# Kernel tuning notes

Hardware: AMD Instinct MI355X
Metric: run time of the kernel (lower is better)

## Reference

```python
import jax, jax.numpy as jnp
import numpy as np
from itertools import permutations

NUM_LAYERS = 3
K = 5  # fixed node degree -> every Hungarian sub-problem is 5x5
# one-hot permutation tensor: P1H[p, r, c] = 1 iff permutation p assigns row r -> col c
PERMS = np.array(list(permutations(range(K))), dtype=np.int32)          # [120, K]
P1H = (PERMS[:, :, None] == np.arange(K)[None, None, :]).astype(np.float32)  # [120, K, K]


def _mlp(x, W1, b1, W2, b2):
    # 2-layer MLP with ReLU (repo's MLP(in, hid, out, 2))
    return jax.nn.relu(x @ W1 + b1) @ W2 + b2


def _sinkhorn(src, itera):
    s = jax.nn.softmax(src, axis=1)  # row-max subtraction is built in
    for i in range(itera):
        s = s / jnp.sum(s, axis=i % 2, keepdims=True)
    return jnp.nan_to_num(s)


def _masked_softmax(src):
    s1 = jnp.nan_to_num(jax.nn.softmax(src, axis=1))
    s2 = jnp.nan_to_num(jax.nn.softmax(src, axis=0))
    return (s1 + s2) * 0.5


def setup_inputs() -> dict:
    key = jax.random.key(0)
    ks = jax.random.split(key, 12)
    n1 = n2 = 1024
    hid = 64
    adj1 = jax.random.randint(ks[0], (n1, K), 0, n1)
    adj2 = jax.random.randint(ks[1], (n2, K), 0, n2)
    # adjacency matrices consistent with the neighbor lists
    G1 = jnp.zeros((n1, n1), jnp.float32).at[jnp.arange(n1)[:, None], adj1].set(1.0)
    G2 = jnp.zeros((n2, n2), jnp.float32).at[jnp.arange(n2)[:, None], adj2].set(1.0)
    s = 0.1
    return {
        'G1': G1, 'G2': G2, 'adj1': adj1, 'adj2': adj2,
        'ro_W1': jax.random.normal(ks[2], (NUM_LAYERS, 1, hid), jnp.float32) * s,
        'ro_b1': jax.random.normal(ks[3], (NUM_LAYERS, hid), jnp.float32) * s,
        'ro_W2': jax.random.normal(ks[4], (NUM_LAYERS, hid, 1), jnp.float32) * s,
        'ro_b2': jax.random.normal(ks[5], (NUM_LAYERS, 1), jnp.float32) * s,
        'fin_W1': jax.random.normal(ks[6], (1, hid), jnp.float32) * s,
        'fin_b1': jax.random.normal(ks[7], (hid,), jnp.float32) * s,
        'fin_W2': jax.random.normal(ks[8], (hid, 1), jnp.float32) * s,
        'fin_b2': jax.random.normal(ks[9], (1,), jnp.float32) * s,
    }


def reference(G1, G2, adj1, adj2, ro_W1, ro_b1, ro_W2, ro_b2, fin_W1, fin_b1, fin_W2, fin_b2):
    n1 = G1.shape[0]
    n2 = G2.shape[0]
    d1 = jnp.sum(G1, axis=1)
    d2 = jnp.sum(G2, axis=1)
    ttheta = jnp.mean(d1)
    # S[i, j, 0] = -|d1[i] - d2[j]|
    S = -jnp.abs(d1[:, None] - d2[None, :])[..., None]  # [n1, n2, 1]
    p1h = jnp.asarray(P1H)
    for li in range(NUM_LAYERS):
        Wn = _sinkhorn(_mlp(S / ttheta, ro_W1[li], ro_b1[li], ro_W2[li], ro_b2[li]).squeeze(-1), 5)
        W = jnp.log(Wn * (n1 * 1.5))
        W = jnp.where(jnp.isneginf(W), jnp.float32(-1e12), W)
        W = jnp.where(jnp.isposinf(W), jnp.float32(1e12), W)
        Wd = jax.lax.stop_gradient(W)  # matches W.detach().numpy()
        # small[a, b, r, c] = Wd[adj1[a, r], adj2[b, c]]  -> [n1, n2, K, K]
        small = jnp.transpose(Wd[adj1][:, :, adj2], (0, 2, 1, 3))
        # exact linear_sum_assignment(-small): maximize sum over the K! permutations
        scores = jnp.einsum('abrc,prc->abp', small, p1h)  # [n1, n2, 120]
        X1 = jnp.max(scores, axis=-1)                      # [n1, n2]
        S = X1[..., None]
    out = _masked_softmax(_mlp(S, fin_W1, fin_b1, fin_W2, fin_b2).squeeze(-1))
    return out
```

## Files before the change

### kernel.cpp

```cpp
#include <hip/hip_runtime.h>
#include <math.h>

#define N 1024
#define NB 256
#define KD 5
#define SL 8


__device__ __forceinline__ float wred_sum(float v){
#pragma unroll
  for (int off = 32; off > 0; off >>= 1) v += __shfl_down(v, off);
  return v;
}
__device__ __forceinline__ float bsum1(float v, float* s64){
  float w = wred_sum(v);
  __syncthreads();
  if ((threadIdx.x & 63) == 0) s64[threadIdx.x >> 6] = w;
  __syncthreads();
  float r = 0.f;
#pragma unroll
  for (int i = 0; i < 16; ++i) r += s64[i];
  return r;
}
__device__ __forceinline__ void bsum4(float v[4], float* s64){
  float w0 = wred_sum(v[0]), w1 = wred_sum(v[1]), w2 = wred_sum(v[2]), w3 = wred_sum(v[3]);
  __syncthreads();
  int wv = threadIdx.x >> 6;
  if ((threadIdx.x & 63) == 0){ s64[wv*4] = w0; s64[wv*4+1] = w1; s64[wv*4+2] = w2; s64[wv*4+3] = w3; }
  __syncthreads();
  float r0 = 0.f, r1 = 0.f, r2 = 0.f, r3 = 0.f;
#pragma unroll
  for (int i = 0; i < 16; ++i){ r0 += s64[i*4]; r1 += s64[i*4+1]; r2 += s64[i*4+2]; r3 += s64[i*4+3]; }
  v[0] = r0; v[1] = r1; v[2] = r2; v[3] = r3;
}

__device__ __forceinline__ int distinct5(const int* v){
  int c = 0;
#pragma unroll
  for (int r = 0; r < KD; ++r){
    bool dup = false;
#pragma unroll
    for (int s = 0; s < r; ++s) dup = dup || (v[s] == v[r]);
    c += dup ? 0 : 1;
  }
  return c;
}

__global__ __launch_bounds__(1024) void
kX1_0(const int* __restrict__ adj1, const int* __restrict__ adj2,
      const float* __restrict__ l0W1, const float* __restrict__ l0B1,
      const float* __restrict__ l0W2, const float* __restrict__ l0B2,
      const float* __restrict__ w1g, const float* __restrict__ b1g,
      const float* __restrict__ w2g, const float* __restrict__ b2g,
      float* __restrict__ tnx, float* __restrict__ CnB, float* __restrict__ ttp)
{
  __shared__ int sd1[N], sd2[N];
  __shared__ int h1[8], h2[8];
  __shared__ float sY[25], slR[5], slC[5], stt[1];
  __shared__ float s64[64];
  __shared__ float ux[64], udA[64], udB[64], xs_s[64], dA_s[64], dB_s[64];
  __shared__ float A_tab[65], B_tab[65], sA0B0[2];
  const int t = threadIdx.x, B = blockIdx.x;

  if (t < 8){ h1[t] = 0; h2[t] = 0; }
  __syncthreads();

  int a2[KD];
#pragma unroll
  for (int c = 0; c < KD; ++c) a2[c] = adj2[t * KD + c];
  int d2v = distinct5(a2);
  sd2[t] = d2v;
  atomicAdd(&h2[d2v - 1], 1);
  {
    int v1[KD];
#pragma unroll
    for (int r = 0; r < KD; ++r) v1[r] = adj1[t * KD + r];
    int d1v = distinct5(v1);
    sd1[t] = d1v;
    atomicAdd(&h1[d1v - 1], 1);
  }
  __syncthreads();

  if (t < 64){
    float cnt1[5], cnt2[5];
#pragma unroll
    for (int g = 0; g < 5; ++g){ cnt1[g] = (float)h1[g]; cnt2[g] = (float)h2[g]; }
    float tt = 0.f;
#pragma unroll
    for (int g = 0; g < 5; ++g) tt += (float)(g + 1) * cnt1[g];
    tt *= (1.0f / 1024.0f);
    float tab[5];
#pragma unroll 1
    for (int i = 0; i < 5; ++i){
      float x = -(float)i / tt;
      float acc = l0B2[0];
      for (int k = 0; k < 64; ++k){
        float hh = fmaxf(fmaf(x, l0W1[k], l0B1[k]), 0.f);
        acc = fmaf(hh, l0W2[k], acc);
      }
      tab[i] = acc;
    }
    float Ee[5][5];
#pragma unroll
    for (int g = 0; g < 5; ++g)
#pragma unroll
      for (int h = 0; h < 5; ++h) Ee[g][h] = expf(tab[abs(g - h)]);
    float q0[5], C1c[5], q1[5], C2c[5], q2[5], C3c[5];
#pragma unroll
    for (int g = 0; g < 5; ++g){
      float s = 0.f;
#pragma unroll
      for (int h = 0; h < 5; ++h) s += cnt2[h] * Ee[g][h];
      q0[g] = s;
    }
#pragma unroll
    for (int h = 0; h < 5; ++h){
      float s = 0.f;
#pragma unroll
      for (int g = 0; g < 5; ++g) s += cnt1[g] * Ee[g][h] / q0[g];
      C1c[h] = s;
    }
#pragma unroll
    for (int g = 0; g < 5; ++g){
      float s = 0.f;
#pragma unroll
      for (int h = 0; h < 5; ++h) s += cnt2[h] * Ee[g][h] / C1c[h];
      q1[g] = s;
    }
#pragma unroll
    for (int h = 0; h < 5; ++h){
      float s = 0.f;
#pragma unroll
      for (int g = 0; g < 5; ++g) s += cnt1[g] * Ee[g][h] / q1[g];
      C2c[h] = s;
    }
#pragma unroll
    for (int g = 0; g < 5; ++g){
      float s = 0.f;
#pragma unroll
      for (int h = 0; h < 5; ++h) s += cnt2[h] * Ee[g][h] / C2c[h];
      q2[g] = s;
    }
#pragma unroll
    for (int h = 0; h < 5; ++h){
      float s = 0.f;
#pragma unroll
      for (int g = 0; g < 5; ++g) s += cnt1[g] * Ee[g][h] / q2[g];
      C3c[h] = s;
    }
    if (t == 0){
#pragma unroll
      for (int g = 0; g < 5; ++g){
#pragma unroll
        for (int h = 0; h < 5; ++h) sY[g * 5 + h] = tab[abs(g - h)];
        slR[g] = -logf(q2[g]);
        slC[g] = logf(C3c[g]);
      }
      stt[0] = tt;
      if (B == 0) ttp[0] = tt;
    }
  } else if (t < 128){
    int l = t - 64;
    float w1 = w1g[l], bb = b1g[l], w2v = w2g[l];
    float xk, sdA, sdB, a0t = 0.f, b0t = 0.f;
    if (w1 != 0.f){
      xk = -bb / w1;
      float dA = w1 * w2v, dB = bb * w2v;
      if (w1 > 0.f){ sdA = dA;  sdB = dB; }
      else         { sdA = -dA; sdB = -dB; a0t = dA; b0t = dB; }
    } else {
      xk = 3.0e38f; sdA = 0.f; sdB = 0.f;
      b0t = fmaxf(bb, 0.f) * w2v;
    }
    ux[l] = xk; udA[l] = sdA; udB[l] = sdB;
    float A0 = wred_sum(a0t);
    float B0 = wred_sum(b0t);
    if (l == 0){ sA0B0[0] = A0; sA0B0[1] = B0 + b2g[0]; }
  }
  __syncthreads();
  if (t < 64){
    float xk = ux[t]; int rank = 0;
    for (int j = 0; j < 64; ++j){
      float xj = ux[j];
      rank += (xj < xk || (xj == xk && j < t)) ? 1 : 0;
    }
    xs_s[rank] = ux[t]; dA_s[rank] = udA[t]; dB_s[rank] = udB[t];
  }
  __syncthreads();
  if (t < 65){
    float sa = sA0B0[0], sb = sA0B0[1];
    for (int r = 0; r < t; ++r){ sa += dA_s[r]; sb += dB_s[r]; }
    A_tab[t] = sa; B_tab[t] = sb;
  }
  __syncthreads();

  const float tt = stt[0];
  const float L1536 = logf(1536.0f);
  int hc[KD];
  float Bvl = 0.f;
#pragma unroll
  for (int c = 0; c < KD; ++c){ hc[c] = sd2[a2[c]] - 1; Bvl -= slC[hc[c]]; }

  float y[4];
#pragma unroll 1
  for (int rr = 0; rr < 4; ++rr){
    float Arow = 5.0f * L1536;
    float f[32];
    f[0] = 0.f;
#pragma unroll
    for (int r = 0; r < KD; ++r){
      int gr = sd1[adj1[(4 * B + rr) * KD + r]] - 1;
      Arow += slR[gr];
      float tr[KD];
#pragma unroll
      for (int c = 0; c < KD; ++c) tr[c] = sY[gr * 5 + hc[c]];
#pragma unroll
      for (int m = 1; m < 32; ++m){
        if (__popc(m) == r + 1){
          float best = -3.0e38f;
#pragma unroll
          for (int c = 0; c < KD; ++c)
            if (m & (1 << c)) best = fmaxf(best, f[m ^ (1 << c)] + tr[c]);
          f[m] = best;
        }
      }
    }
    float X1v = Arow + Bvl + f[31];
    float x = X1v / tt;
    int seg = 0;
#pragma unroll
    for (int s = 64; s; s >>= 1)
      if (seg + s <= 64 && xs_s[seg + s - 1] <= x) seg += s;
    y[rr] = fmaf(A_tab[seg], x, B_tab[seg]);
  }
  float e4[4], q4[4];
#pragma unroll
  for (int r = 0; r < 4; ++r){
    tnx[(size_t)(4 * B + r) * N + t] = y[r];
    e4[r] = expf(y[r]);
    q4[r] = e4[r];
  }
  bsum4(q4, s64);
  float cp = 0.f;
#pragma unroll
  for (int r = 0; r < 4; ++r) cp += e4[r] / q4[r];
  atomicAdd(&CnB[(size_t)(B & (SL - 1)) * N + t], cp);
}

__global__ __launch_bounds__(1024) void
kS(const float* __restrict__ tm, const float* __restrict__ CinB, float* __restrict__ CoutB,
   float* __restrict__ Rg, int writeRg)
{
  __shared__ float s64[64];
  const int t = threadIdx.x, B = blockIdx.x;
  float C = 0.f;
#pragma unroll
  for (int k = 0; k < SL; ++k) C += CinB[(size_t)k * N + t];
  float iC = 1.0f / C;
  float e[4], q[4];
#pragma unroll
  for (int r = 0; r < 4; ++r){
    e[r] = expf(tm[(size_t)(4 * B + r) * N + t]);
    q[r] = e[r] * iC;
  }
  bsum4(q, s64);
  float cp = 0.f;
#pragma unroll
  for (int r = 0; r < 4; ++r) cp += e[r] / q[r];
  atomicAdd(&CoutB[(size_t)(B & (SL - 1)) * N + t], cp);
  if (writeRg && t < 4) Rg[4 * B + t] = 1.0f / q[t];
}

__global__ __launch_bounds__(1024) void
kX1(const float* __restrict__ tm, const int* __restrict__ adj1, const int* __restrict__ adj2,
    const float* __restrict__ ttp, const float* __restrict__ Rg, const float* __restrict__ C3B,
    const float* __restrict__ w1g, const float* __restrict__ b1g,
    const float* __restrict__ w2g, const float* __restrict__ b2g,
    int isFinal, float* __restrict__ tnx, float* __restrict__ CoutB,
    float* __restrict__ rsF)
{
  __shared__ __align__(16) float rows20[20][N];
  __shared__ float lc[N];
  __shared__ float s64[64];
  __shared__ float sAv[4];
  __shared__ float ux[64], udA[64], udB[64], xs_s[64], dA_s[64], dB_s[64];
  __shared__ float A_tab[65], B_tab[65], sA0B0[2];
  const int t = threadIdx.x, B = blockIdx.x;

  const float tt = ttp[0];
  int a2[KD];
#pragma unroll
  for (int c = 0; c < KD; ++c) a2[c] = adj2[t * KD + c];

  {
    int w = t >> 6, lane = t & 63;
    int seg = w & 3;
    int rbase = w >> 2;
#pragma unroll
    for (int k = 0; k < 5; ++k){
      int r2 = rbase + 4 * k;
      int src = adj1[(4 * B + (r2 / 5)) * KD + (r2 % 5)];
      const float* g = tm + (size_t)src * N + seg * 256 + lane * 4;
      __builtin_amdgcn_global_load_lds(
          (const __attribute__((address_space(1))) unsigned int*)g,
          (__attribute__((address_space(3))) unsigned int*)&rows20[r2][seg * 256],
          16, 0, 0);
    }
  }
  {
    float C = 0.f;
#pragma unroll
    for (int k = 0; k < SL; ++k) C += C3B[(size_t)k * N + t];
    lc[t] = logf(C);
  }
  if (t >= 64 && t < 68){
    int a = 4 * B + (t - 64);
    float s = 5.0f * logf(1536.0f);
#pragma unroll
    for (int r = 0; r < KD; ++r) s += logf(Rg[adj1[a * KD + r]]);
    sAv[t - 64] = s;
  }
  if (t < 64){
    float w1 = w1g[t], bb = b1g[t], w2 = w2g[t];
    float xk, sdA, sdB, a0t = 0.f, b0t = 0.f;
    if (w1 != 0.f){
      xk = -bb / w1;
      float dA = w1 * w2, dB = bb * w2;
      if (w1 > 0.f){ sdA = dA;  sdB = dB; }
      else         { sdA = -dA; sdB = -dB; a0t = dA; b0t = dB; }
    } else {
      xk = 3.0e38f; sdA = 0.f; sdB = 0.f;
      b0t = fmaxf(bb, 0.f) * w2;
    }
    ux[t] = xk; udA[t] = sdA; udB[t] = sdB;
    float A0 = wred_sum(a0t);
    float B0 = wred_sum(b0t);
    if (t == 0){ sA0B0[0] = A0; sA0B0[1] = B0 + b2g[0]; }
  }
  __syncthreads();
  if (t < 64){
    float xk = ux[t]; int rank = 0;
    for (int j = 0; j < 64; ++j){
      float xj = ux[j];
      rank += (xj < xk || (xj == xk && j < t)) ? 1 : 0;
    }
    xs_s[rank] = ux[t]; dA_s[rank] = udA[t]; dB_s[rank] = udB[t];
  }
  __syncthreads();
  if (t < 65){
    float sa = sA0B0[0], sb = sA0B0[1];
    for (int r = 0; r < t; ++r){ sa += dA_s[r]; sb += dB_s[r]; }
    A_tab[t] = sa; B_tab[t] = sb;
  }
  __syncthreads();

  float Bvl = 0.f;
#pragma unroll
  for (int c = 0; c < KD; ++c) Bvl -= lc[a2[c]];

  float y[4];
#pragma unroll 1
  for (int rr = 0; rr < 4; ++rr){
    float f[32];
    f[0] = 0.f;
#pragma unroll
    for (int r = 0; r < KD; ++r){
      float tr[KD];
#pragma unroll
      for (int c = 0; c < KD; ++c) tr[c] = rows20[rr * 5 + r][a2[c]];
#pragma unroll
      for (int m = 1; m < 32; ++m){
        if (__popc(m) == r + 1){
          float best = -3.0e38f;
#pragma unroll
          for (int c = 0; c < KD; ++c)
            if (m & (1 << c)) best = fmaxf(best, f[m ^ (1 << c)] + tr[c]);
          f[m] = best;
        }
      }
    }
    float X1v = sAv[rr] + Bvl + f[31];
    float x = isFinal ? X1v : (X1v / tt);
    int seg = 0;
#pragma unroll
    for (int s = 64; s; s >>= 1)
      if (seg + s <= 64 && xs_s[seg + s - 1] <= x) seg += s;
    y[rr] = fmaf(A_tab[seg], x, B_tab[seg]);
  }

  float e4[4], q4[4];
#pragma unroll
  for (int r = 0; r < 4; ++r){ e4[r] = expf(y[r]); q4[r] = e4[r]; }
  bsum4(q4, s64);

  float cp = 0.f;
#pragma unroll
  for (int r = 0; r < 4; ++r){
    tnx[(size_t)(4 * B + r) * N + t] = y[r];
    cp += isFinal ? e4[r] : (e4[r] / q4[r]);
  }
  atomicAdd(&CoutB[(size_t)(B & (SL - 1)) * N + t], cp);
  if (isFinal && t < 4) rsF[4 * B + t] = q4[t];
}

__global__ __launch_bounds__(1024) void
k_combine(const float* __restrict__ y, const float* __restrict__ rsF,
          const float* __restrict__ CFB, float* __restrict__ out)
{
  const int t = threadIdx.x, B = blockIdx.x;
  float CF = 0.f;
#pragma unroll
  for (int k = 0; k < SL; ++k) CF += CFB[(size_t)k * N + t];
  float iCF = 1.0f / CF;
#pragma unroll
  for (int r = 0; r < 4; ++r){
    int a = 4 * B + r;
    float ev = expf(y[(size_t)a * N + t]);
    out[(size_t)a * N + t] = 0.5f * ev * (1.0f / rsF[a] + iCF);
  }
}

extern "C" void kernel_launch(void* const* d_in, const int* in_sizes, int n_in,
                              void* d_out, int out_size, void* d_ws, size_t ws_size,
                              hipStream_t stream){
  (void)in_sizes; (void)n_in; (void)out_size; (void)ws_size;
  const int*   adj1 = (const int*)d_in[2];
  const int*   adj2 = (const int*)d_in[3];
  const float* roW1 = (const float*)d_in[4];
  const float* roB1 = (const float*)d_in[5];
  const float* roW2 = (const float*)d_in[6];
  const float* roB2 = (const float*)d_in[7];
  const float* fW1  = (const float*)d_in[8];
  const float* fB1  = (const float*)d_in[9];
  const float* fW2  = (const float*)d_in[10];
  const float* fB2  = (const float*)d_in[11];
  float* out = (float*)d_out;

  float* wsA = (float*)d_ws;
  float* Pp  = wsA + (size_t)N * N;
  float* Rg  = Pp + (size_t)7 * SL * N;
  float* rsF = Rg + N;
  float* ttp = rsF + N;

  kX1_0<<<NB, 1024, 0, stream>>>(adj1, adj2, roW1, roB1, roW2, roB2,
                                 roW1 + 64, roB1 + 64, roW2 + 64, roB2 + 1,
                                 wsA, Pp, ttp);
  kS<<<NB, 1024, 0, stream>>>(wsA, Pp + (size_t)0 * SL * N, Pp + (size_t)1 * SL * N, Rg, 0);
  kS<<<NB, 1024, 0, stream>>>(wsA, Pp + (size_t)1 * SL * N, Pp + (size_t)2 * SL * N, Rg, 1);
  kX1<<<NB, 1024, 0, stream>>>(wsA, adj1, adj2, ttp, Rg, Pp + (size_t)2 * SL * N,
                               roW1 + 128, roB1 + 128, roW2 + 128, roB2 + 2,
                               0, out, Pp + (size_t)3 * SL * N, rsF);
  kS<<<NB, 1024, 0, stream>>>(out, Pp + (size_t)3 * SL * N, Pp + (size_t)4 * SL * N, Rg, 0);
  kS<<<NB, 1024, 0, stream>>>(out, Pp + (size_t)4 * SL * N, Pp + (size_t)5 * SL * N, Rg, 1);
  kX1<<<NB, 1024, 0, stream>>>(out, adj1, adj2, ttp, Rg, Pp + (size_t)5 * SL * N,
                               fW1, fB1, fW2, fB2,
                               1, wsA, Pp + (size_t)6 * SL * N, rsF);
  k_combine<<<NB, 1024, 0, stream>>>(wsA, rsF, Pp + (size_t)6 * SL * N, out);
}
```

Baseline: 163.3 us.

## Fuse per-layer Sinkhorn and assignment kernels with software grid barriers

```diff
diff --git a/kernel.cpp b/kernel.cpp
--- a/kernel.cpp
+++ b/kernel.cpp
@@ -5,22 +5,48 @@
 #define NB 256
 #define KD 5
 #define SL 8
-
+#define MAGIC 0x13572468
+#define FSTRIDE 32
+#define FREGION (NB * FSTRIDE + FSTRIDE)
+
+
+__device__ __forceinline__ float load_sc(const float* p){
+  return __hip_atomic_load(p, __ATOMIC_RELAXED, __HIP_MEMORY_SCOPE_AGENT);
+}
+__device__ __forceinline__ void store_sc(float* p, float v){
+  __hip_atomic_store(p, v, __ATOMIC_RELAXED, __HIP_MEMORY_SCOPE_AGENT);
+}
+__device__ __forceinline__ int load_sci(const int* p){
+  return __hip_atomic_load(p, __ATOMIC_RELAXED, __HIP_MEMORY_SCOPE_AGENT);
+}
+__device__ __forceinline__ void store_sci(int* p, int v){
+  __hip_atomic_store(p, v, __ATOMIC_RELAXED, __HIP_MEMORY_SCOPE_AGENT);
+}
+
+__device__ __forceinline__ void gbarS(int* flg){
+  __builtin_amdgcn_s_waitcnt(0);
+  __syncthreads();
+  const int t = threadIdx.x, B = blockIdx.x;
+  int* go = flg + NB * FSTRIDE;
+  if (B == 0){
+    if (t > 0 && t < NB){
+      while (load_sci(&flg[t * FSTRIDE]) != MAGIC) __builtin_amdgcn_s_sleep(2);
+    }
+    __syncthreads();
+    if (t == 0) store_sci(go, MAGIC);
+  } else {
+    if (t == 0){
+      store_sci(&flg[B * FSTRIDE], MAGIC);
+      while (load_sci(go) != MAGIC) __builtin_amdgcn_s_sleep(2);
+    }
+    __syncthreads();
+  }
+}
 
 __device__ __forceinline__ float wred_sum(float v){
 #pragma unroll
   for (int off = 32; off > 0; off >>= 1) v += __shfl_down(v, off);
   return v;
-}
-__device__ __forceinline__ float bsum1(float v, float* s64){
-  float w = wred_sum(v);
-  __syncthreads();
-  if ((threadIdx.x & 63) == 0) s64[threadIdx.x >> 6] = w;
-  __syncthreads();
-  float r = 0.f;
-#pragma unroll
-  for (int i = 0; i < 16; ++i) r += s64[i];
-  return r;
 }
 __device__ __forceinline__ void bsum4(float v[4], float* s64){
   float w0 = wred_sum(v[0]), w1 = wred_sum(v[1]), w2 = wred_sum(v[2]), w3 = wred_sum(v[3]);
@@ -248,36 +274,14 @@
 }
 
 __global__ __launch_bounds__(1024) void
-kS(const float* __restrict__ tm, const float* __restrict__ CinB, float* __restrict__ CoutB,
-   float* __restrict__ Rg, int writeRg)
-{
-  __shared__ float s64[64];
-  const int t = threadIdx.x, B = blockIdx.x;
-  float C = 0.f;
-#pragma unroll
-  for (int k = 0; k < SL; ++k) C += CinB[(size_t)k * N + t];
-  float iC = 1.0f / C;
-  float e[4], q[4];
-#pragma unroll
-  for (int r = 0; r < 4; ++r){
-    e[r] = expf(tm[(size_t)(4 * B + r) * N + t]);
-    q[r] = e[r] * iC;
-  }
-  bsum4(q, s64);
-  float cp = 0.f;
-#pragma unroll
-  for (int r = 0; r < 4; ++r) cp += e[r] / q[r];
-  atomicAdd(&CoutB[(size_t)(B & (SL - 1)) * N + t], cp);
-  if (writeRg && t < 4) Rg[4 * B + t] = 1.0f / q[t];
-}
-
-__global__ __launch_bounds__(1024) void
-kX1(const float* __restrict__ tm, const int* __restrict__ adj1, const int* __restrict__ adj2,
-    const float* __restrict__ ttp, const float* __restrict__ Rg, const float* __restrict__ C3B,
-    const float* __restrict__ w1g, const float* __restrict__ b1g,
-    const float* __restrict__ w2g, const float* __restrict__ b2g,
-    int isFinal, float* __restrict__ tnx, float* __restrict__ CoutB,
-    float* __restrict__ rsF)
+kLayer(const float* __restrict__ tm, const int* __restrict__ adj1, const int* __restrict__ adj2,
+       const float* __restrict__ ttp,
+       const float* __restrict__ C1B, float* __restrict__ C2B, float* __restrict__ C3B,
+       float* __restrict__ CnB, float* __restrict__ Rg,
+       const float* __restrict__ w1g, const float* __restrict__ b1g,
+       const float* __restrict__ w2g, const float* __restrict__ b2g,
+       int isFinal, float* __restrict__ tnx,
+       int* __restrict__ bar1, int* __restrict__ bar2, int* __restrict__ bar3)
 {
   __shared__ __align__(16) float rows20[20][N];
   __shared__ float lc[N];
@@ -307,19 +311,10 @@
           16, 0, 0);
     }
   }
-  {
-    float C = 0.f;
-#pragma unroll
-    for (int k = 0; k < SL; ++k) C += C3B[(size_t)k * N + t];
-    lc[t] = logf(C);
-  }
-  if (t >= 64 && t < 68){
-    int a = 4 * B + (t - 64);
-    float s = 5.0f * logf(1536.0f);
-#pragma unroll
-    for (int r = 0; r < KD; ++r) s += logf(Rg[adj1[a * KD + r]]);
-    sAv[t - 64] = s;
-  }
+  float E[4], q4[4];
+#pragma unroll
+  for (int r = 0; r < 4; ++r) E[r] = expf(tm[(size_t)(4 * B + r) * N + t]);
+
   if (t < 64){
     float w1 = w1g[t], bb = b1g[t], w2 = w2g[t];
     float xk, sdA, sdB, a0t = 0.f, b0t = 0.f;
@@ -352,6 +347,51 @@
     for (int r = 0; r < t; ++r){ sa += dA_s[r]; sb += dB_s[r]; }
     A_tab[t] = sa; B_tab[t] = sb;
   }
+
+  {
+    float C = 0.f;
+#pragma unroll
+    for (int k = 0; k < SL; ++k) C += C1B[(size_t)k * N + t];
+    float iC = 1.0f / C;
+#pragma unroll
+    for (int r = 0; r < 4; ++r) q4[r] = E[r] * iC;
+    bsum4(q4, s64);
+    float cp = 0.f;
+#pragma unroll
+    for (int r = 0; r < 4; ++r) cp += E[r] / q4[r];
+    atomicAdd(&C2B[(size_t)(B & (SL - 1)) * N + t], cp);
+  }
+
+  gbarS(bar1);
+  {
+    float C = 0.f;
+#pragma unroll
+    for (int k = 0; k < SL; ++k) C += load_sc(&C2B[(size_t)k * N + t]);
+    float iC = 1.0f / C;
+#pragma unroll
+    for (int r = 0; r < 4; ++r) q4[r] = E[r] * iC;
+    bsum4(q4, s64);
+    float cp = 0.f;
+#pragma unroll
+    for (int r = 0; r < 4; ++r) cp += E[r] / q4[r];
+    if (t < 4) store_sc(&Rg[4 * B + t], 1.0f / q4[t]);
+    atomicAdd(&C3B[(size_t)(B & (SL - 1)) * N + t], cp);
+  }
+
+  gbarS(bar2);
+  {
+    float C = 0.f;
+#pragma unroll
+    for (int k = 0; k < SL; ++k) C += load_sc(&C3B[(size_t)k * N + t]);
+    lc[t] = logf(C);
+  }
+  if (t >= 64 && t < 68){
+    int a = 4 * B + (t - 64);
+    float s = 5.0f * logf(1536.0f);
+#pragma unroll
+    for (int r = 0; r < KD; ++r) s += logf(load_sc(&Rg[adj1[a * KD + r]]));
+    sAv[t - 64] = s;
+  }
   __syncthreads();
 
   float Bvl = 0.f;
@@ -388,35 +428,34 @@
     y[rr] = fmaf(A_tab[seg], x, B_tab[seg]);
   }
 
-  float e4[4], q4[4];
+  float e4[4];
 #pragma unroll
   for (int r = 0; r < 4; ++r){ e4[r] = expf(y[r]); q4[r] = e4[r]; }
   bsum4(q4, s64);
 
-  float cp = 0.f;
-#pragma unroll
-  for (int r = 0; r < 4; ++r){
-    tnx[(size_t)(4 * B + r) * N + t] = y[r];
-    cp += isFinal ? e4[r] : (e4[r] / q4[r]);
-  }
-  atomicAdd(&CoutB[(size_t)(B & (SL - 1)) * N + t], cp);
-  if (isFinal && t < 4) rsF[4 * B + t] = q4[t];
-}
-
-__global__ __launch_bounds__(1024) void
-k_combine(const float* __restrict__ y, const float* __restrict__ rsF,
-          const float* __restrict__ CFB, float* __restrict__ out)
-{
-  const int t = threadIdx.x, B = blockIdx.x;
-  float CF = 0.f;
-#pragma unroll
-  for (int k = 0; k < SL; ++k) CF += CFB[(size_t)k * N + t];
-  float iCF = 1.0f / CF;
-#pragma unroll
-  for (int r = 0; r < 4; ++r){
-    int a = 4 * B + r;
-    float ev = expf(y[(size_t)a * N + t]);
-    out[(size_t)a * N + t] = 0.5f * ev * (1.0f / rsF[a] + iCF);
+  if (!isFinal){
+    float cp = 0.f;
+#pragma unroll
+    for (int r = 0; r < 4; ++r){
+      tnx[(size_t)(4 * B + r) * N + t] = y[r];
+      cp += e4[r] / q4[r];
+    }
+    atomicAdd(&CnB[(size_t)(B & (SL - 1)) * N + t], cp);
+  } else {
+    float cp = 0.f;
+#pragma unroll
+    for (int r = 0; r < 4; ++r) cp += e4[r];
+    atomicAdd(&CnB[(size_t)(B & (SL - 1)) * N + t], cp);
+    gbarS(bar3);
+    float CF = 0.f;
+#pragma unroll
+    for (int k = 0; k < SL; ++k) CF += load_sc(&CnB[(size_t)k * N + t]);
+    float iCF = 1.0f / CF;
+#pragma unroll
+    for (int r = 0; r < 4; ++r){
+      float v = 0.5f * e4[r] * (1.0f / q4[r] + iCF);
+      tnx[(size_t)(4 * B + r) * N + t] = v;
+    }
   }
 }
 
@@ -439,21 +478,22 @@
   float* wsA = (float*)d_ws;
   float* Pp  = wsA + (size_t)N * N;
   float* Rg  = Pp + (size_t)7 * SL * N;
-  float* rsF = Rg + N;
-  float* ttp = rsF + N;
+  float* ttp = Rg + N;
+  int*   flg = (int*)(ttp + 8);
 
   kX1_0<<<NB, 1024, 0, stream>>>(adj1, adj2, roW1, roB1, roW2, roB2,
                                  roW1 + 64, roB1 + 64, roW2 + 64, roB2 + 1,
                                  wsA, Pp, ttp);
-  kS<<<NB, 1024, 0, stream>>>(wsA, Pp + (size_t)0 * SL * N, Pp + (size_t)1 * SL * N, Rg, 0);
-  kS<<<NB, 1024, 0, stream>>>(wsA, Pp + (size_t)1 * SL * N, Pp + (size_t)2 * SL * N, Rg, 1);
-  kX1<<<NB, 1024, 0, stream>>>(wsA, adj1, adj2, ttp, Rg, Pp + (size_t)2 * SL * N,
-                               roW1 + 128, roB1 + 128, roW2 + 128, roB2 + 2,
-                               0, out, Pp + (size_t)3 * SL * N, rsF);
-  kS<<<NB, 1024, 0, stream>>>(out, Pp + (size_t)3 * SL * N, Pp + (size_t)4 * SL * N, Rg, 0);
-  kS<<<NB, 1024, 0, stream>>>(out, Pp + (size_t)4 * SL * N, Pp + (size_t)5 * SL * N, Rg, 1);
-  kX1<<<NB, 1024, 0, stream>>>(out, adj1, adj2, ttp, Rg, Pp + (size_t)5 * SL * N,
-                               fW1, fB1, fW2, fB2,
-                               1, wsA, Pp + (size_t)6 * SL * N, rsF);
-  k_combine<<<NB, 1024, 0, stream>>>(wsA, rsF, Pp + (size_t)6 * SL * N, out);
-}
+  kLayer<<<NB, 1024, 0, stream>>>(wsA, adj1, adj2, ttp,
+                                  Pp + (size_t)0 * SL * N, Pp + (size_t)1 * SL * N,
+                                  Pp + (size_t)2 * SL * N, Pp + (size_t)3 * SL * N, Rg,
+                                  roW1 + 128, roB1 + 128, roW2 + 128, roB2 + 2,
+                                  0, out,
+                                  flg + 0 * FREGION, flg + 1 * FREGION, flg + 2 * FREGION);
+  kLayer<<<NB, 1024, 0, stream>>>(out, adj1, adj2, ttp,
+                                  Pp + (size_t)3 * SL * N, Pp + (size_t)4 * SL * N,
+                                  Pp + (size_t)5 * SL * N, Pp + (size_t)6 * SL * N, Rg,
+                                  fW1, fB1, fW2, fB2,
+                                  1, out,
+                                  flg + 2 * FREGION, flg + 3 * FREGION, flg + 4 * FREGION);
+}
```

Result: no change. 161.9 us (-0.9%).
